# Optimization experiments

Hardware: AMD Instinct MI355X
Metric: run time of the kernel (lower is better)

Reference implementation:

```python
import jax, jax.numpy as jnp
import numpy as np

Q = 128          # number of slices
S = 1024 // Q    # slice length = 8
U = 32           # hidden units per slice
EPS = 1e-3       # keras LayerNormalization default epsilon


def setup_inputs() -> dict:
    key = jax.random.key(0)
    ks = jax.random.split(key, 8)
    B = 16384
    x = jax.random.normal(ks[0], (B, 1, 1, Q * S), dtype=jnp.float32)
    # per-slice Dense1 (S->U), LayerNorm(gamma,beta), Dense2 (U->1)
    W1 = jax.random.normal(ks[1], (Q, S, U), dtype=jnp.float32) / np.sqrt(S)
    b1 = jnp.zeros((Q, U), dtype=jnp.float32)
    gamma = jnp.ones((Q, U), dtype=jnp.float32)
    beta = jnp.zeros((Q, U), dtype=jnp.float32)
    W2 = jax.random.normal(ks[2], (Q, U), dtype=jnp.float32) / np.sqrt(U)
    b2 = jnp.zeros((Q,), dtype=jnp.float32)
    return {"x": x, "W1": W1, "b1": b1, "gamma": gamma, "beta": beta,
            "W2": W2, "b2": b2}


def reference(x, W1, b1, gamma, beta, W2, b2):
    B = x.shape[0]
    xs = x.reshape(B, Q, S)                              # (B,Q,S)
    # batched tiny Dense -> ELU
    h = jnp.einsum('bqs,qsu->bqu', xs, W1) + b1          # (B,Q,U)
    h = jax.nn.elu(h)
    # per-slice LayerNorm over last axis
    mu = jnp.mean(h, axis=-1, keepdims=True)
    var = jnp.mean(jnp.square(h - mu), axis=-1, keepdims=True)
    h = (h - mu) * jax.lax.rsqrt(var + EPS) * gamma + beta
    # batched output projection U -> 1, concat over slices
    out = jnp.einsum('bqu,qu->bq', h, W2) + b2           # (B,Q)
    return out
```

## Files before the change

### kernel.cpp

```cpp
#include <hip/hip_runtime.h>


typedef __attribute__((ext_vector_type(8))) short short8;
typedef __attribute__((ext_vector_type(16))) float f32x16;

#define XS_STRIDE 40

__device__ __forceinline__ short fbits(__bf16 b) { return __builtin_bit_cast(short, b); }

__device__ __forceinline__ float elu1(float v) {
    return v > 0.f ? v : __expf(v) - 1.f;
}

__device__ __forceinline__ short4 cvt4(float4 v) {
    short4 r;
    r.x = fbits((__bf16)v.x); r.y = fbits((__bf16)v.y);
    r.z = fbits((__bf16)v.z); r.w = fbits((__bf16)v.w);
    return r;
}

__device__ __forceinline__ void barrier_ds_only() {
    asm volatile("s_waitcnt lgkmcnt(0)" ::: "memory");
    __builtin_amdgcn_s_barrier();
}

__global__ __launch_bounds__(256, 4) void divenc_mfma(
    const float* __restrict__ x,
    const float* __restrict__ W1,
    const float* __restrict__ b1,
    const float* __restrict__ gamma,
    const float* __restrict__ beta,
    const float* __restrict__ W2,
    const float* __restrict__ b2,
    float* __restrict__ out)
{
    __shared__ short xs[3][64 * XS_STRIDE];
    __shared__ float lout[512 * 5];

    const int tid  = threadIdx.x;
    const int w    = tid >> 6;
    const int ln   = tid & 63;
    const int u    = ln & 31;
    const int half = ln >> 5;
    const int qt   = blockIdx.y;
    const int q    = qt * 4 + w;
    const int bx   = blockIdx.x;
    const int band = bx * 512;

    const int srow0 = tid >> 3;
    const int srow1 = srow0 + 32;
    const int schk  = tid & 7;
    const float* xpan = x + qt * 32 + schk * 4;

    short8 wfrag;
    #pragma unroll
    for (int j = 0; j < 8; ++j) {
        float f  = W1[q * 256 + j * 32 + u];
        __bf16 h = (__bf16)f;
        wfrag[j] = half ? fbits((__bf16)(f - (float)h)) : fbits(h);
    }

    f32x16 biasr, g2r;
    float G, C;
    {
        float gs = 0.f, cs = 0.f;
        #pragma unroll
        for (int c = 0; c < 4; ++c) {
            const int ub = q * 32 + 4 * half + 8 * c;
            float4 b1v = *(const float4*)&b1[ub];
            float4 gav = *(const float4*)&gamma[ub];
            float4 w2v = *(const float4*)&W2[ub];
            float4 bev = *(const float4*)&beta[ub];
            #pragma unroll
            for (int j = 0; j < 4; ++j) {
                float g2 = ((const float*)&gav)[j] * ((const float*)&w2v)[j];
                biasr[4 * c + j] = ((const float*)&b1v)[j];
                g2r[4 * c + j]   = g2;
                gs += g2;
                cs += ((const float*)&bev)[j] * ((const float*)&w2v)[j];
            }
        }
        gs += __shfl_xor(gs, 32);
        cs += __shfl_xor(cs, 32);
        G = gs;
        C = cs + b2[q];
    }

    {
        float4 g0 = *(const float4*)(xpan + (size_t)(band + srow0) * 1024);
        float4 g1 = *(const float4*)(xpan + (size_t)(band + srow1) * 1024);
        *(short4*)&xs[0][srow0 * XS_STRIDE + schk * 4] = cvt4(g0);
        *(short4*)&xs[0][srow1 * XS_STRIDE + schk * 4] = cvt4(g1);
    }
    float4 p0 = *(const float4*)(xpan + (size_t)(band + 64 + srow0) * 1024);
    float4 p1 = *(const float4*)(xpan + (size_t)(band + 64 + srow1) * 1024);
    barrier_ds_only();

    #pragma unroll 1
    for (int it = 0; it < 8; ++it) {
        const int cur = it % 3;
        const int nxt = (it + 1) % 3;
        const int b0  = it * 64;

        float4 f0, f1;
        if (it < 6) {
            f0 = *(const float4*)(xpan + (size_t)(band + b0 + 128 + srow0) * 1024);
            f1 = *(const float4*)(xpan + (size_t)(band + b0 + 128 + srow1) * 1024);
        }

        short8 xa = *(const short8*)&xs[cur][u * XS_STRIDE + w * 8];
        short8 xb = *(const short8*)&xs[cur][(u + 32) * XS_STRIDE + w * 8];

        f32x16 accA = __builtin_amdgcn_mfma_f32_32x32x16_bf16(wfrag, xa, biasr, 0, 0, 0);
        f32x16 accB = __builtin_amdgcn_mfma_f32_32x32x16_bf16(wfrag, xb, biasr, 0, 0, 0);

        {
            float sum = 0.f, ss = 0.f, dot = 0.f;
            #pragma unroll
            for (int r = 0; r < 16; ++r) {
                float e = elu1(accA[r]);
                sum += e;
                ss  = fmaf(e, e, ss);
                dot = fmaf(e, g2r[r], dot);
            }
            sum += __shfl_xor(sum, 32);
            ss  += __shfl_xor(ss, 32);
            dot += __shfl_xor(dot, 32);
            float mu  = sum * 0.03125f;
            float var = fmaf(-mu, mu, ss * 0.03125f);
            float inv = rsqrtf(var + 1e-3f);
            float res = fmaf(inv, fmaf(-mu, G, dot), C);
            if (half == 0) lout[(b0 + u) * 5 + w] = res;
        }
        {
            float sum = 0.f, ss = 0.f, dot = 0.f;
            #pragma unroll
            for (int r = 0; r < 16; ++r) {
                float e = elu1(accB[r]);
                sum += e;
                ss  = fmaf(e, e, ss);
                dot = fmaf(e, g2r[r], dot);
            }
            sum += __shfl_xor(sum, 32);
            ss  += __shfl_xor(ss, 32);
            dot += __shfl_xor(dot, 32);
            float mu  = sum * 0.03125f;
            float var = fmaf(-mu, mu, ss * 0.03125f);
            float inv = rsqrtf(var + 1e-3f);
            float res = fmaf(inv, fmaf(-mu, G, dot), C);
            if (half == 0) lout[(b0 + 32 + u) * 5 + w] = res;
        }

        if (it < 7) {
            *(short4*)&xs[nxt][srow0 * XS_STRIDE + schk * 4] = cvt4(p0);
            *(short4*)&xs[nxt][srow1 * XS_STRIDE + schk * 4] = cvt4(p1);
            barrier_ds_only();
        }

        p0 = f0;
        p1 = f1;
    }

    __syncthreads();

    {
        const int r0 = tid;
        const int r1 = tid + 256;
        float4 o0, o1;
        o0.x = lout[r0 * 5 + 0]; o0.y = lout[r0 * 5 + 1];
        o0.z = lout[r0 * 5 + 2]; o0.w = lout[r0 * 5 + 3];
        o1.x = lout[r1 * 5 + 0]; o1.y = lout[r1 * 5 + 1];
        o1.z = lout[r1 * 5 + 2]; o1.w = lout[r1 * 5 + 3];
        *(float4*)(out + (size_t)(band + r0) * 128 + qt * 4) = o0;
        *(float4*)(out + (size_t)(band + r1) * 128 + qt * 4) = o1;
    }
}

extern "C" void kernel_launch(void* const* d_in, const int* in_sizes, int n_in,
                              void* d_out, int out_size, void* d_ws, size_t ws_size,
                              hipStream_t stream) {
    const float* x     = (const float*)d_in[0];
    const float* W1    = (const float*)d_in[1];
    const float* b1    = (const float*)d_in[2];
    const float* gamma = (const float*)d_in[3];
    const float* beta  = (const float*)d_in[4];
    const float* W2    = (const float*)d_in[5];
    const float* b2    = (const float*)d_in[6];
    float* out = (float*)d_out;

    dim3 grid(32, 32);
    divenc_mfma<<<grid, 256, 0, stream>>>(x, W1, b1, gamma, beta, W2, b2, out);
}
```

Baseline: 27.64 us.

## Warp-specialize with a dedicated producer wave loading x tiles into LDS

Adds a fifth wavefront per block that only issues global loads of x, converts them to bf16 and writes them into the triple-buffered LDS ring. The four compute waves now only do the MFMA, ELU and LayerNorm epilogue. The intent is to take global-load latency and conversion work off the compute waves and overlap them through the shared barriers. The cost is that a single wave issues all the loads with more registers in flight (16 float4 per lane), and the barrier count rises on the compute path, which could serialize loading.

After: 29.12 us. 1.05x slower.

```diff
diff --git a/kernel.cpp b/kernel.cpp
--- a/kernel.cpp
+++ b/kernel.cpp
@@ -24,7 +24,7 @@
     __builtin_amdgcn_s_barrier();
 }
 
-__global__ __launch_bounds__(256, 4) void divenc_mfma(
+__global__ __launch_bounds__(320, 4) void divenc_ws(
     const float* __restrict__ x,
     const float* __restrict__ W1,
     const float* __restrict__ b1,
@@ -43,127 +43,137 @@
     const int u    = ln & 31;
     const int half = ln >> 5;
     const int qt   = blockIdx.y;
-    const int q    = qt * 4 + w;
     const int bx   = blockIdx.x;
     const int band = bx * 512;
 
-    const int srow0 = tid >> 3;
-    const int srow1 = srow0 + 32;
-    const int schk  = tid & 7;
-    const float* xpan = x + qt * 32 + schk * 4;
-
-    short8 wfrag;
-    #pragma unroll
-    for (int j = 0; j < 8; ++j) {
-        float f  = W1[q * 256 + j * 32 + u];
-        __bf16 h = (__bf16)f;
-        wfrag[j] = half ? fbits((__bf16)(f - (float)h)) : fbits(h);
+    if (w == 4) {
+        const int prow = ln >> 3;
+        const int chk  = ln & 7;
+        const float* xg = x + qt * 32 + chk * 4;
+
+        float4 A[8], Bv[8];
+        #pragma unroll
+        for (int j = 0; j < 8; ++j)
+            A[j] = *(const float4*)(xg + (size_t)(band + j * 8 + prow) * 1024);
+        #pragma unroll
+        for (int j = 0; j < 8; ++j)
+            Bv[j] = *(const float4*)(xg + (size_t)(band + 64 + j * 8 + prow) * 1024);
+        #pragma unroll
+        for (int j = 0; j < 8; ++j)
+            *(short4*)&xs[0][(j * 8 + prow) * XS_STRIDE + chk * 4] = cvt4(A[j]);
+        barrier_ds_only();
+
+        #pragma unroll 1
+        for (int it = 0; it < 8; ++it) {
+            const int pn = (it + 2 > 7) ? 7 : (it + 2);
+            float4 N[8];
+            #pragma unroll
+            for (int j = 0; j < 8; ++j)
+                N[j] = *(const float4*)(xg + (size_t)(band + pn * 64 + j * 8 + prow) * 1024);
+            if (it < 7) {
+                short* dst = &xs[(it + 1) % 3][0];
+                #pragma unroll
+                for (int j = 0; j < 8; ++j)
+                    *(short4*)&dst[(j * 8 + prow) * XS_STRIDE + chk * 4] = cvt4(Bv[j]);
+            }
+            barrier_ds_only();
+            #pragma unroll
+            for (int j = 0; j < 8; ++j) Bv[j] = N[j];
+        }
+    } else {
+        const int q = qt * 4 + w;
+
+        short8 wfrag;
+        #pragma unroll
+        for (int j = 0; j < 8; ++j) {
+            float f  = W1[q * 256 + j * 32 + u];
+            __bf16 h = (__bf16)f;
+            wfrag[j] = half ? fbits((__bf16)(f - (float)h)) : fbits(h);
+        }
+
+        f32x16 biasr, g2r;
+        float G, C;
+        {
+            float gs = 0.f, cs = 0.f;
+            #pragma unroll
+            for (int c = 0; c < 4; ++c) {
+                const int ub = q * 32 + 4 * half + 8 * c;
+                float4 b1v = *(const float4*)&b1[ub];
+                float4 gav = *(const float4*)&gamma[ub];
+                float4 w2v = *(const float4*)&W2[ub];
+                float4 bev = *(const float4*)&beta[ub];
+                #pragma unroll
+                for (int j = 0; j < 4; ++j) {
+                    float g2 = ((const float*)&gav)[j] * ((const float*)&w2v)[j];
+                    biasr[4 * c + j] = ((const float*)&b1v)[j];
+                    g2r[4 * c + j]   = g2;
+                    gs += g2;
+                    cs += ((const float*)&bev)[j] * ((const float*)&w2v)[j];
+                }
+            }
+            gs += __shfl_xor(gs, 32);
+            cs += __shfl_xor(cs, 32);
+            G = gs;
+            C = cs + b2[q];
+        }
+
+        barrier_ds_only();
+
+        #pragma unroll 1
+        for (int it = 0; it < 8; ++it) {
+            const int cur = it % 3;
+            const int b0  = it * 64;
+
+            short8 xa = *(const short8*)&xs[cur][u * XS_STRIDE + w * 8];
+            short8 xb = *(const short8*)&xs[cur][(u + 32) * XS_STRIDE + w * 8];
+
+            f32x16 accA = __builtin_amdgcn_mfma_f32_32x32x16_bf16(wfrag, xa, biasr, 0, 0, 0);
+            f32x16 accB = __builtin_amdgcn_mfma_f32_32x32x16_bf16(wfrag, xb, biasr, 0, 0, 0);
+
+            {
+                float sum = 0.f, ss = 0.f, dot = 0.f;
+                #pragma unroll
+                for (int r = 0; r < 16; ++r) {
+                    float e = elu1(accA[r]);
+                    sum += e;
+                    ss  = fmaf(e, e, ss);
+                    dot = fmaf(e, g2r[r], dot);
+                }
+                sum += __shfl_xor(sum, 32);
+                ss  += __shfl_xor(ss, 32);
+                dot += __shfl_xor(dot, 32);
+                float mu  = sum * 0.03125f;
+                float var = fmaf(-mu, mu, ss * 0.03125f);
+                float inv = rsqrtf(var + 1e-3f);
+                float res = fmaf(inv, fmaf(-mu, G, dot), C);
+                if (half == 0) lout[(b0 + u) * 5 + w] = res;
+            }
+            {
+                float sum = 0.f, ss = 0.f, dot = 0.f;
+                #pragma unroll
+                for (int r = 0; r < 16; ++r) {
+                    float e = elu1(accB[r]);
+                    sum += e;
+                    ss  = fmaf(e, e, ss);
+                    dot = fmaf(e, g2r[r], dot);
+                }
+                sum += __shfl_xor(sum, 32);
+                ss  += __shfl_xor(ss, 32);
+                dot += __shfl_xor(dot, 32);
+                float mu  = sum * 0.03125f;
+                float var = fmaf(-mu, mu, ss * 0.03125f);
+                float inv = rsqrtf(var + 1e-3f);
+                float res = fmaf(inv, fmaf(-mu, G, dot), C);
+                if (half == 0) lout[(b0 + 32 + u) * 5 + w] = res;
+            }
+
+            barrier_ds_only();
+        }
     }
 
-    f32x16 biasr, g2r;
-    float G, C;
-    {
-        float gs = 0.f, cs = 0.f;
-        #pragma unroll
-        for (int c = 0; c < 4; ++c) {
-            const int ub = q * 32 + 4 * half + 8 * c;
-            float4 b1v = *(const float4*)&b1[ub];
-            float4 gav = *(const float4*)&gamma[ub];
-            float4 w2v = *(const float4*)&W2[ub];
-            float4 bev = *(const float4*)&beta[ub];
-            #pragma unroll
-            for (int j = 0; j < 4; ++j) {
-                float g2 = ((const float*)&gav)[j] * ((const float*)&w2v)[j];
-                biasr[4 * c + j] = ((const float*)&b1v)[j];
-                g2r[4 * c + j]   = g2;
-                gs += g2;
-                cs += ((const float*)&bev)[j] * ((const float*)&w2v)[j];
-            }
-        }
-        gs += __shfl_xor(gs, 32);
-        cs += __shfl_xor(cs, 32);
-        G = gs;
-        C = cs + b2[q];
-    }
-
-    {
-        float4 g0 = *(const float4*)(xpan + (size_t)(band + srow0) * 1024);
-        float4 g1 = *(const float4*)(xpan + (size_t)(band + srow1) * 1024);
-        *(short4*)&xs[0][srow0 * XS_STRIDE + schk * 4] = cvt4(g0);
-        *(short4*)&xs[0][srow1 * XS_STRIDE + schk * 4] = cvt4(g1);
-    }
-    float4 p0 = *(const float4*)(xpan + (size_t)(band + 64 + srow0) * 1024);
-    float4 p1 = *(const float4*)(xpan + (size_t)(band + 64 + srow1) * 1024);
-    barrier_ds_only();
-
-    #pragma unroll 1
-    for (int it = 0; it < 8; ++it) {
-        const int cur = it % 3;
-        const int nxt = (it + 1) % 3;
-        const int b0  = it * 64;
-
-        float4 f0, f1;
-        if (it < 6) {
-            f0 = *(const float4*)(xpan + (size_t)(band + b0 + 128 + srow0) * 1024);
-            f1 = *(const float4*)(xpan + (size_t)(band + b0 + 128 + srow1) * 1024);
-        }
-
-        short8 xa = *(const short8*)&xs[cur][u * XS_STRIDE + w * 8];
-        short8 xb = *(const short8*)&xs[cur][(u + 32) * XS_STRIDE + w * 8];
-
-        f32x16 accA = __builtin_amdgcn_mfma_f32_32x32x16_bf16(wfrag, xa, biasr, 0, 0, 0);
-        f32x16 accB = __builtin_amdgcn_mfma_f32_32x32x16_bf16(wfrag, xb, biasr, 0, 0, 0);
-
-        {
-            float sum = 0.f, ss = 0.f, dot = 0.f;
-            #pragma unroll
-            for (int r = 0; r < 16; ++r) {
-                float e = elu1(accA[r]);
-                sum += e;
-                ss  = fmaf(e, e, ss);
-                dot = fmaf(e, g2r[r], dot);
-            }
-            sum += __shfl_xor(sum, 32);
-            ss  += __shfl_xor(ss, 32);
-            dot += __shfl_xor(dot, 32);
-            float mu  = sum * 0.03125f;
-            float var = fmaf(-mu, mu, ss * 0.03125f);
-            float inv = rsqrtf(var + 1e-3f);
-            float res = fmaf(inv, fmaf(-mu, G, dot), C);
-            if (half == 0) lout[(b0 + u) * 5 + w] = res;
-        }
-        {
-            float sum = 0.f, ss = 0.f, dot = 0.f;
-            #pragma unroll
-            for (int r = 0; r < 16; ++r) {
-                float e = elu1(accB[r]);
-                sum += e;
-                ss  = fmaf(e, e, ss);
-                dot = fmaf(e, g2r[r], dot);
-            }
-            sum += __shfl_xor(sum, 32);
-            ss  += __shfl_xor(ss, 32);
-            dot += __shfl_xor(dot, 32);
-            float mu  = sum * 0.03125f;
-            float var = fmaf(-mu, mu, ss * 0.03125f);
-            float inv = rsqrtf(var + 1e-3f);
-            float res = fmaf(inv, fmaf(-mu, G, dot), C);
-            if (half == 0) lout[(b0 + 32 + u) * 5 + w] = res;
-        }
-
-        if (it < 7) {
-            *(short4*)&xs[nxt][srow0 * XS_STRIDE + schk * 4] = cvt4(p0);
-            *(short4*)&xs[nxt][srow1 * XS_STRIDE + schk * 4] = cvt4(p1);
-            barrier_ds_only();
-        }
-
-        p0 = f0;
-        p1 = f1;
-    }
-
     __syncthreads();
 
-    {
+    if (tid < 256) {
         const int r0 = tid;
         const int r1 = tid + 256;
         float4 o0, o1;
@@ -189,5 +199,5 @@
     float* out = (float*)d_out;
 
     dim3 grid(32, 32);
-    divenc_mfma<<<grid, 256, 0, stream>>>(x, W1, b1, gamma, beta, W2, b2, out);
-}
+    divenc_ws<<<grid, 320, 0, stream>>>(x, W1, b1, gamma, beta, W2, b2, out);
+}
```

## Halve rows per block, defer LayerNorm finalize to epilogue, vectorize ELU

Applied to the files above, without the earlier changes.

Each block now handles 256 batch rows instead of 512, which doubles the grid to 64x32 and shortens the per-block loop to 4 iterations. Partial sums for mean, sum of squares and the W2 dot product are written to shared memory per half-wavefront. This replaces the in-loop cross-lane shuffles, and one epilogue pass finishes the LayerNorm and output for every row. The ELU is rewritten branch-free with max/min on packed float2 so the compiler can use packed FP32 ops. The cost is more blocks that each redo the weight setup, more shared memory, and a barrier on every iteration.

New measurement: 28.94 us. +4.7%, slower.

```diff
diff --git a/kernel.cpp b/kernel.cpp
--- a/kernel.cpp
+++ b/kernel.cpp
@@ -3,14 +3,11 @@
 
 typedef __attribute__((ext_vector_type(8))) short short8;
 typedef __attribute__((ext_vector_type(16))) float f32x16;
+typedef __attribute__((ext_vector_type(2)))  float f32x2;
 
 #define XS_STRIDE 40
 
 __device__ __forceinline__ short fbits(__bf16 b) { return __builtin_bit_cast(short, b); }
-
-__device__ __forceinline__ float elu1(float v) {
-    return v > 0.f ? v : __expf(v) - 1.f;
-}
 
 __device__ __forceinline__ short4 cvt4(float4 v) {
     short4 r;
@@ -35,7 +32,8 @@
     float* __restrict__ out)
 {
     __shared__ short xs[3][64 * XS_STRIDE];
-    __shared__ float lout[512 * 5];
+    __shared__ float pl[3][2][4][256];
+    __shared__ float GC[4][2];
 
     const int tid  = threadIdx.x;
     const int w    = tid >> 6;
@@ -45,7 +43,7 @@
     const int qt   = blockIdx.y;
     const int q    = qt * 4 + w;
     const int bx   = blockIdx.x;
-    const int band = bx * 512;
+    const int band = bx * 256;
 
     const int srow0 = tid >> 3;
     const int srow1 = srow0 + 32;
@@ -61,7 +59,6 @@
     }
 
     f32x16 biasr, g2r;
-    float G, C;
     {
         float gs = 0.f, cs = 0.f;
         #pragma unroll
@@ -82,8 +79,10 @@
         }
         gs += __shfl_xor(gs, 32);
         cs += __shfl_xor(cs, 32);
-        G = gs;
-        C = cs + b2[q];
+        if (ln == 0) {
+            GC[w][0] = gs;
+            GC[w][1] = cs + b2[q];
+        }
     }
 
     {
@@ -96,14 +95,17 @@
     float4 p1 = *(const float4*)(xpan + (size_t)(band + 64 + srow1) * 1024);
     barrier_ds_only();
 
+    const f32x2 zero2 = {0.f, 0.f};
+    const f32x2 one2  = {1.f, 1.f};
+
     #pragma unroll 1
-    for (int it = 0; it < 8; ++it) {
+    for (int it = 0; it < 4; ++it) {
         const int cur = it % 3;
         const int nxt = (it + 1) % 3;
         const int b0  = it * 64;
 
         float4 f0, f1;
-        if (it < 6) {
+        if (it < 2) {
             f0 = *(const float4*)(xpan + (size_t)(band + b0 + 128 + srow0) * 1024);
             f1 = *(const float4*)(xpan + (size_t)(band + b0 + 128 + srow1) * 1024);
         }
@@ -114,48 +116,35 @@
         f32x16 accA = __builtin_amdgcn_mfma_f32_32x32x16_bf16(wfrag, xa, biasr, 0, 0, 0);
         f32x16 accB = __builtin_amdgcn_mfma_f32_32x32x16_bf16(wfrag, xb, biasr, 0, 0, 0);
 
-        {
-            float sum = 0.f, ss = 0.f, dot = 0.f;
+        #pragma unroll
+        for (int t = 0; t < 2; ++t) {
+            const f32x16& acc = t ? accB : accA;
+            f32x2 vs = zero2, vq = zero2, vd = zero2;
             #pragma unroll
-            for (int r = 0; r < 16; ++r) {
-                float e = elu1(accA[r]);
-                sum += e;
-                ss  = fmaf(e, e, ss);
-                dot = fmaf(e, g2r[r], dot);
+            for (int i = 0; i < 8; ++i) {
+                f32x2 va = { acc[2 * i], acc[2 * i + 1] };
+                f32x2 g2 = { g2r[2 * i], g2r[2 * i + 1] };
+                f32x2 mx = __builtin_elementwise_max(va, zero2);
+                f32x2 mn = __builtin_elementwise_min(va, zero2);
+                f32x2 ex;
+                ex.x = __expf(mn.x);
+                ex.y = __expf(mn.y);
+                f32x2 e = mx + (ex - one2);
+                vs += e;
+                vq += e * e;
+                vd += e * g2;
             }
-            sum += __shfl_xor(sum, 32);
-            ss  += __shfl_xor(ss, 32);
-            dot += __shfl_xor(dot, 32);
-            float mu  = sum * 0.03125f;
-            float var = fmaf(-mu, mu, ss * 0.03125f);
-            float inv = rsqrtf(var + 1e-3f);
-            float res = fmaf(inv, fmaf(-mu, G, dot), C);
-            if (half == 0) lout[(b0 + u) * 5 + w] = res;
-        }
-        {
-            float sum = 0.f, ss = 0.f, dot = 0.f;
-            #pragma unroll
-            for (int r = 0; r < 16; ++r) {
-                float e = elu1(accB[r]);
-                sum += e;
-                ss  = fmaf(e, e, ss);
-                dot = fmaf(e, g2r[r], dot);
-            }
-            sum += __shfl_xor(sum, 32);
-            ss  += __shfl_xor(ss, 32);
-            dot += __shfl_xor(dot, 32);
-            float mu  = sum * 0.03125f;
-            float var = fmaf(-mu, mu, ss * 0.03125f);
-            float inv = rsqrtf(var + 1e-3f);
-            float res = fmaf(inv, fmaf(-mu, G, dot), C);
-            if (half == 0) lout[(b0 + 32 + u) * 5 + w] = res;
+            const int row = b0 + t * 32 + u;
+            pl[0][half][w][row] = vs.x + vs.y;
+            pl[1][half][w][row] = vq.x + vq.y;
+            pl[2][half][w][row] = vd.x + vd.y;
         }
 
-        if (it < 7) {
+        if (it < 3) {
             *(short4*)&xs[nxt][srow0 * XS_STRIDE + schk * 4] = cvt4(p0);
             *(short4*)&xs[nxt][srow1 * XS_STRIDE + schk * 4] = cvt4(p1);
-            barrier_ds_only();
         }
+        barrier_ds_only();
 
         p0 = f0;
         p1 = f1;
@@ -164,15 +153,18 @@
     __syncthreads();
 
     {
-        const int r0 = tid;
-        const int r1 = tid + 256;
-        float4 o0, o1;
-        o0.x = lout[r0 * 5 + 0]; o0.y = lout[r0 * 5 + 1];
-        o0.z = lout[r0 * 5 + 2]; o0.w = lout[r0 * 5 + 3];
-        o1.x = lout[r1 * 5 + 0]; o1.y = lout[r1 * 5 + 1];
-        o1.z = lout[r1 * 5 + 2]; o1.w = lout[r1 * 5 + 3];
-        *(float4*)(out + (size_t)(band + r0) * 128 + qt * 4) = o0;
-        *(float4*)(out + (size_t)(band + r1) * 128 + qt * 4) = o1;
+        float4 o;
+        #pragma unroll
+        for (int q4 = 0; q4 < 4; ++q4) {
+            float sum = pl[0][0][q4][tid] + pl[0][1][q4][tid];
+            float ss  = pl[1][0][q4][tid] + pl[1][1][q4][tid];
+            float dot = pl[2][0][q4][tid] + pl[2][1][q4][tid];
+            float mu  = sum * 0.03125f;
+            float var = fmaf(-mu, mu, ss * 0.03125f);
+            float inv = rsqrtf(var + 1e-3f);
+            ((float*)&o)[q4] = fmaf(inv, fmaf(-mu, GC[q4][0], dot), GC[q4][1]);
+        }
+        *(float4*)(out + (size_t)(band + tid) * 128 + qt * 4) = o;
     }
 }
 
@@ -188,6 +180,6 @@
     const float* b2    = (const float*)d_in[6];
     float* out = (float*)d_out;
 
-    dim3 grid(32, 32);
+    dim3 grid(64, 32);
     divenc_mfma<<<grid, 256, 0, stream>>>(x, W1, b1, gamma, beta, W2, b2, out);
 }
```

## Pair cross-half reductions and defer LayerNorm finalize to next iteration

Applied to the files above, without the earlier changes.

Each half-wave keeps its own partial sums for one of the two 32-row tiles and exchanges only the other tile's partials, so three shuffles replace six and all 64 lanes write an output. The finalize (shuffle, rsqrt, store) for a tile is moved into the next iteration, behind that iteration's MFMAs, with a tail step after the loop. The aim is to cut cross-lane traffic and hide shuffle latency, at the cost of carrying six extra live registers across iterations.

Measured after the change: 30.87 us. +11.7%, slower.

```diff
diff --git a/kernel.cpp b/kernel.cpp
--- a/kernel.cpp
+++ b/kernel.cpp
@@ -96,6 +96,9 @@
     float4 p1 = *(const float4*)(xpan + (size_t)(band + 64 + srow1) * 1024);
     barrier_ds_only();
 
+    float dKs = 0.f, dKq = 0.f, dKd = 0.f;
+    float dSs = 0.f, dSq = 0.f, dSd = 0.f;
+
     #pragma unroll 1
     for (int it = 0; it < 8; ++it) {
         const int cur = it % 3;
@@ -114,42 +117,30 @@
         f32x16 accA = __builtin_amdgcn_mfma_f32_32x32x16_bf16(wfrag, xa, biasr, 0, 0, 0);
         f32x16 accB = __builtin_amdgcn_mfma_f32_32x32x16_bf16(wfrag, xb, biasr, 0, 0, 0);
 
-        {
-            float sum = 0.f, ss = 0.f, dot = 0.f;
-            #pragma unroll
-            for (int r = 0; r < 16; ++r) {
-                float e = elu1(accA[r]);
-                sum += e;
-                ss  = fmaf(e, e, ss);
-                dot = fmaf(e, g2r[r], dot);
-            }
-            sum += __shfl_xor(sum, 32);
-            ss  += __shfl_xor(ss, 32);
-            dot += __shfl_xor(dot, 32);
-            float mu  = sum * 0.03125f;
-            float var = fmaf(-mu, mu, ss * 0.03125f);
+        if (it > 0) {
+            float ts = dKs + __shfl_xor(dSs, 32);
+            float tq = dKq + __shfl_xor(dSq, 32);
+            float td = dKd + __shfl_xor(dSd, 32);
+            float mu  = ts * 0.03125f;
+            float var = fmaf(-mu, mu, tq * 0.03125f);
             float inv = rsqrtf(var + 1e-3f);
-            float res = fmaf(inv, fmaf(-mu, G, dot), C);
-            if (half == 0) lout[(b0 + u) * 5 + w] = res;
+            float res = fmaf(inv, fmaf(-mu, G, td), C);
+            lout[(b0 - 64 + ln) * 5 + w] = res;
         }
-        {
-            float sum = 0.f, ss = 0.f, dot = 0.f;
-            #pragma unroll
-            for (int r = 0; r < 16; ++r) {
-                float e = elu1(accB[r]);
-                sum += e;
-                ss  = fmaf(e, e, ss);
-                dot = fmaf(e, g2r[r], dot);
-            }
-            sum += __shfl_xor(sum, 32);
-            ss  += __shfl_xor(ss, 32);
-            dot += __shfl_xor(dot, 32);
-            float mu  = sum * 0.03125f;
-            float var = fmaf(-mu, mu, ss * 0.03125f);
-            float inv = rsqrtf(var + 1e-3f);
-            float res = fmaf(inv, fmaf(-mu, G, dot), C);
-            if (half == 0) lout[(b0 + 32 + u) * 5 + w] = res;
+
+        float sA = 0.f, qA = 0.f, dA = 0.f;
+        float sB = 0.f, qB = 0.f, dB = 0.f;
+        #pragma unroll
+        for (int r = 0; r < 16; ++r) {
+            float eA = elu1(accA[r]);
+            float eB = elu1(accB[r]);
+            sA += eA;                    sB += eB;
+            qA = fmaf(eA, eA, qA);       qB = fmaf(eB, eB, qB);
+            dA = fmaf(eA, g2r[r], dA);   dB = fmaf(eB, g2r[r], dB);
         }
+        float nKs = half ? sB : sA, nSs = half ? sA : sB;
+        float nKq = half ? qB : qA, nSq = half ? qA : qB;
+        float nKd = half ? dB : dA, nSd = half ? dA : dB;
 
         if (it < 7) {
             *(short4*)&xs[nxt][srow0 * XS_STRIDE + schk * 4] = cvt4(p0);
@@ -157,8 +148,21 @@
             barrier_ds_only();
         }
 
+        dKs = nKs; dKq = nKq; dKd = nKd;
+        dSs = nSs; dSq = nSq; dSd = nSd;
         p0 = f0;
         p1 = f1;
+    }
+
+    {
+        float ts = dKs + __shfl_xor(dSs, 32);
+        float tq = dKq + __shfl_xor(dSq, 32);
+        float td = dKd + __shfl_xor(dSd, 32);
+        float mu  = ts * 0.03125f;
+        float var = fmaf(-mu, mu, tq * 0.03125f);
+        float inv = rsqrtf(var + 1e-3f);
+        float res = fmaf(inv, fmaf(-mu, G, td), C);
+        lout[(448 + ln) * 5 + w] = res;
     }
 
     __syncthreads();
```
